# Kernel optimization log

Hardware: AMD Instinct MI355X
Metric: run time of the kernel (lower is better)

## Reference

```python
import jax, jax.numpy as jnp
import numpy as np

NUM_CLASSES = 1203
C = NUM_CLASSES + 1
ITER = 9001            # > warm_up_iter=8000 (full path), not a multiple of save_iter=1000
GAMMA = 1.0
BETA = 1.0             # forward default loss_type=1 -> beta = 1
EMA = 0.999
LOWER = 1.0 / 3.0
UPPER = 5.0
LOSS_WEIGHT_ARG = 1.0  # forward `loss_weight` arg default
SELF_LOSS_WEIGHT = 1.0 # __init__ loss_weight
N = 16384              # multiple of 64 (interval in collect_grad_optim)


def setup_inputs() -> dict:
    key = jax.random.key(0)
    k1, k2, k3, k4, k5 = jax.random.split(key, 5)
    cls_score = jax.random.normal(k1, (N, C), jnp.float32)
    label = jax.random.randint(k2, (N,), 0, C)
    weight = jax.random.uniform(k3, (N,), jnp.float32)
    classes_logits = jax.random.normal(k4, (C,), jnp.float32) * 0.01
    class_weights_buf = jnp.ones((C,), jnp.float32)
    corr_grad_accu = jax.random.normal(k5, (C, C), jnp.float32) * 0.01
    weights_mean = jnp.ones((1,), jnp.float32)
    return {"cls_score": cls_score, "label": label, "weight": weight,
            "classes_logits": classes_logits, "class_weights_buf": class_weights_buf,
            "corr_grad_accu": corr_grad_accu, "weights_mean": weights_mean}


def reference(cls_score, label, weight, classes_logits, class_weights_buf,
              corr_grad_accu, weights_mean):
    sg = jax.lax.stop_gradient
    n = cls_score.shape[0]
    target = jax.nn.one_hot(label, C, dtype=cls_score.dtype)  # expand_label

    # ---- get_weight (no_grad in torch): beta=1, iter % save_iter != 0 ----
    cw = jnp.clip(class_weights_buf, LOWER, UPPER)
    tmp_weight = (cw ** BETA)[label]                 # (class_weights**beta * target).sum(1)
    wm = EMA * weights_mean[0] + (1.0 - EMA) * tmp_weight.mean()
    tmp_weight = tmp_weight / wm
    tmp_weight = sg(tmp_weight * weight)             # detached in torch

    # ---- focal cross-entropy ----
    logp = jax.nn.log_softmax(cls_score, axis=-1)
    CE = -jnp.take_along_axis(logp, label[:, None], axis=1)[:, 0]
    p = jnp.exp(-CE)
    loss = (1.0 - p) ** GAMMA * CE
    loss = (loss * tmp_weight).mean()                # weight_reduce_loss mean

    # ---- collect_grad_optim (all under no_grad in torch) ----
    cs = sg(cls_score)
    w = sg(weight)
    prob = jax.nn.softmax(cs, axis=-1) + 1e-5                       # [N,C]
    focal_grad = w[:, None] * ((1.0 - prob) / prob - jnp.log(prob)) # [N,C]
    pos_grad = ((1.0 - prob) * prob * focal_grad * target).mean(0)  # [C]
    # corr[i,j] = mean_n target[n,i]*focal_grad[n,i]*prob[n,i]*prob[n,j]
    a = target * focal_grad * prob                                  # [N,C]
    corr = jnp.einsum('ni,nj->ij', a, prob) / n                     # [C,C]
    diag = jnp.arange(C)
    corr = corr.at[diag, diag].set(-pos_grad)
    corr_grad = corr * 100.0 * LOSS_WEIGHT_ARG      # dist.all_reduce = identity (1 proc)

    # ITER >= warm_up_iter branch: EMA update + class weights from logits
    accu = EMA * sg(corr_grad_accu) + (1.0 - EMA) * corr_grad
    cw2 = sg(jax.nn.softmax(classes_logits)) * C    # detached in torch

    tcw = (cw2[:, None] * accu).sum(0) / (-jnp.diagonal(accu) + 1e-6) + cw2
    # ITER > warm_up_iter branch:
    tcw = tcw.at[-1].set(C - tcw[:-1].sum())
    tcw = jnp.clip(tcw, LOWER, UPPER)
    tcw = tcw.at[-1].set(jnp.clip(tcw[-1], LOWER, 1.0))
    tcw = sg(jnp.log(tcw))
    loss_grad = ((tcw - classes_logits) ** 2).mean()

    return (SELF_LOSS_WEIGHT * loss, loss_grad, cw2)
```

## Files before the change

kernel.cpp:

```cpp
#include <hip/hip_runtime.h>
#include <math.h>

#define C_  1204
#define C4_ 301
#define NROWBLK 2048

__device__ __forceinline__ float waveReduceSum(float v){
    #pragma unroll
    for (int o = 32; o > 0; o >>= 1) v += __shfl_xor(v, o, 64);
    return v;
}
__device__ __forceinline__ float exp4(float4 v){
    return __expf(v.x) + __expf(v.y) + __expf(v.z) + __expf(v.w);
}
__device__ __forceinline__ float4 accExp(float4 acc, float sc, float4 x){
    acc.x += sc * __expf(x.x); acc.y += sc * __expf(x.y);
    acc.z += sc * __expf(x.z); acc.w += sc * __expf(x.w);
    return acc;
}

__global__ void k_init(float* posg, int* counts, float* tcol){
    int i = blockIdx.x * blockDim.x + threadIdx.x;
    if (i < C_){ posg[i] = 0.f; counts[i] = 0; tcol[i] = 0.f; }
}

__global__ void k_rows(const float* __restrict__ cs, const int* __restrict__ label,
                       const float* __restrict__ w, const float* __restrict__ cwb,
                       float* __restrict__ rowsum, float* __restrict__ aN,
                       float* posg, int* counts,
                       float* __restrict__ part1, float* __restrict__ part2){
    int lane = threadIdx.x & 63;
    int wid  = threadIdx.x >> 6;
    int nA = (blockIdx.x * 4 + wid) * 2;
    int nB = nA + 1;
    const float4* rowA = reinterpret_cast<const float4*>(cs + (size_t)nA * C_);
    const float4* rowB = reinterpret_cast<const float4*>(cs + (size_t)nB * C_);
    bool has4 = lane < (C4_ - 256);

    float4 a0 = rowA[lane], a1 = rowA[lane + 64], a2 = rowA[lane + 128], a3 = rowA[lane + 192];
    float4 b0 = rowB[lane], b1 = rowB[lane + 64], b2 = rowB[lane + 128], b3 = rowB[lane + 192];
    float4 a4, b4;
    if (has4){ a4 = rowA[lane + 256]; b4 = rowB[lane + 256]; }

    float sA = exp4(a0) + exp4(a1) + exp4(a2) + exp4(a3);
    float sB = exp4(b0) + exp4(b1) + exp4(b2) + exp4(b3);
    if (has4){ sA += exp4(a4); sB += exp4(b4); }
    sA = waveReduceSum(sA);
    sB = waveReduceSum(sB);

    __shared__ float lr1[8], lr2[8];
    if (lane < 2){
        int   n = (lane == 0) ? nA : nB;
        float s = (lane == 0) ? sA : sB;
        rowsum[n] = s;
        int l = label[n];
        float x = cs[(size_t)n * C_ + l];
        float logp = x - __logf(s);
        float p = __expf(logp);
        float lossc = (1.f - p) * (-logp);
        float t = fminf(fmaxf(cwb[l], 1.f/3.f), 5.f);
        float wn = w[n];
        float pp = p + 1e-5f;
        float fg = wn * ((1.f - pp) / pp - __logf(pp));
        aN[n] = fg * pp;
        atomicAdd(&posg[l], (1.f - pp) * pp * fg);
        atomicAdd(&counts[l], 1);
        lr1[wid * 2 + lane] = lossc * t * wn;
        lr2[wid * 2 + lane] = t;
    }
    __syncthreads();
    if (threadIdx.x == 0){
        float s1 = 0.f, s2 = 0.f;
        #pragma unroll
        for (int k = 0; k < 8; ++k){ s1 += lr1[k]; s2 += lr2[k]; }
        part1[blockIdx.x] = s1;
        part2[blockIdx.x] = s2;
    }
}

__global__ void k_mid(const int* __restrict__ counts, int* offsets, int* cursor,
                      const float* __restrict__ logits, float* cw2, float* out){
    __shared__ int partial[256];
    __shared__ float red[256];
    int t = threadIdx.x;
    int base = t * 5;
    int local[5]; int s = 0;
    #pragma unroll
    for (int k = 0; k < 5; ++k){
        int idx = base + k;
        int c = (idx < C_) ? counts[idx] : 0;
        local[k] = s; s += c;
    }
    partial[t] = s;
    __syncthreads();
    for (int o = 1; o < 256; o <<= 1){
        int v = 0;
        if (t >= o) v = partial[t - o];
        __syncthreads();
        partial[t] += v;
        __syncthreads();
    }
    int pre = (t > 0) ? partial[t - 1] : 0;
    #pragma unroll
    for (int k = 0; k < 5; ++k){
        int idx = base + k;
        if (idx < C_){ offsets[idx] = pre + local[k]; cursor[idx] = pre + local[k]; }
    }

    float x[5]; float m = -3.402823466e38f;
    #pragma unroll
    for (int k = 0; k < 5; ++k){
        int j = t + k * 256;
        x[k] = (j < C_) ? logits[j] : -3.402823466e38f;
        m = fmaxf(m, x[k]);
    }
    red[t] = m; __syncthreads();
    for (int o = 128; o > 0; o >>= 1){ if (t < o) red[t] = fmaxf(red[t], red[t+o]); __syncthreads(); }
    float bm = red[0]; __syncthreads();
    float ss = 0.f;
    #pragma unroll
    for (int k = 0; k < 5; ++k){ int j = t + k * 256; if (j < C_) ss += __expf(x[k] - bm); }
    red[t] = ss; __syncthreads();
    for (int o = 128; o > 0; o >>= 1){ if (t < o) red[t] += red[t+o]; __syncthreads(); }
    float bs = red[0]; __syncthreads();
    #pragma unroll
    for (int k = 0; k < 5; ++k){
        int j = t + k * 256;
        if (j < C_){ float v = __expf(x[k] - bm) / bs * (float)C_; cw2[j] = v; out[2 + j] = v; }
    }
}

__global__ void k_scatter(const int* __restrict__ label, int* cursor, int* bucket){
    int n = blockIdx.x * blockDim.x + threadIdx.x;
    int l = label[n];
    int pos = atomicAdd(&cursor[l], 1);
    bucket[pos] = n;
}

__global__ void k_corr(const float* __restrict__ cs, const int* __restrict__ bucket,
                       const int* __restrict__ counts, const int* __restrict__ offsets,
                       const float* __restrict__ rowsum, const float* __restrict__ aN,
                       const float* __restrict__ posg, const float* __restrict__ cga,
                       float* __restrict__ accu, int Nn){
    int i = blockIdx.x;
    int t = threadIdx.x;
    int cnt = counts[i], start = offsets[i];
    bool has2 = t < (C4_ - 256);
    float4 acc0 = {0.f,0.f,0.f,0.f}, acc1 = {0.f,0.f,0.f,0.f};
    float suma = 0.f;

    int nbat = (cnt + 7) >> 3;
    for (int b = 0; b < nbat; ++b){
        int s = b << 3;
        #define LOADR(k) \
            int  id##k = min(s + k, cnt - 1); \
            int  n##k  = bucket[start + id##k]; \
            float va##k = aN[n##k]; \
            float iv##k = (s + k < cnt) ? va##k / rowsum[n##k] : 0.f; \
            float ma##k = (s + k < cnt) ? va##k : 0.f; \
            const float4* rp##k = reinterpret_cast<const float4*>(cs + (size_t)n##k * C_); \
            float4 x0##k = rp##k[t]; \
            float4 x1##k; if (has2) x1##k = rp##k[t + 256];
        LOADR(0) LOADR(1) LOADR(2) LOADR(3) LOADR(4) LOADR(5) LOADR(6) LOADR(7)
        #undef LOADR
        suma += ma0 + ma1 + ma2 + ma3 + ma4 + ma5 + ma6 + ma7;
        acc0 = accExp(acc0, iv0, x00); acc0 = accExp(acc0, iv1, x01);
        acc0 = accExp(acc0, iv2, x02); acc0 = accExp(acc0, iv3, x03);
        acc0 = accExp(acc0, iv4, x04); acc0 = accExp(acc0, iv5, x05);
        acc0 = accExp(acc0, iv6, x06); acc0 = accExp(acc0, iv7, x07);
        if (has2){
            acc1 = accExp(acc1, iv0, x10); acc1 = accExp(acc1, iv1, x11);
            acc1 = accExp(acc1, iv2, x12); acc1 = accExp(acc1, iv3, x13);
            acc1 = accExp(acc1, iv4, x14); acc1 = accExp(acc1, iv5, x15);
            acc1 = accExp(acc1, iv6, x16); acc1 = accExp(acc1, iv7, x17);
        }
    }

    float eps   = suma * 1e-5f;
    float scale = 100.f / (float)Nn;
    float diagv = -100.f * posg[i] / (float)Nn;
    const float4* cga4 = reinterpret_cast<const float4*>(cga + (size_t)i * C_);
    float4*       out4 = reinterpret_cast<float4*>(accu + (size_t)i * C_);
    int d4 = i >> 2, dc = i & 3;

    float4 cgv;
    cgv.x = (acc0.x + eps) * scale; cgv.y = (acc0.y + eps) * scale;
    cgv.z = (acc0.z + eps) * scale; cgv.w = (acc0.w + eps) * scale;
    if (t == d4){
        if (dc == 0) cgv.x = diagv; else if (dc == 1) cgv.y = diagv;
        else if (dc == 2) cgv.z = diagv; else cgv.w = diagv;
    }
    float4 gv = cga4[t];
    float4 wv;
    wv.x = 0.999f*gv.x + 0.001f*cgv.x; wv.y = 0.999f*gv.y + 0.001f*cgv.y;
    wv.z = 0.999f*gv.z + 0.001f*cgv.z; wv.w = 0.999f*gv.w + 0.001f*cgv.w;
    out4[t] = wv;

    if (has2){
        int t2 = t + 256;
        float4 cgv1;
        cgv1.x = (acc1.x + eps) * scale; cgv1.y = (acc1.y + eps) * scale;
        cgv1.z = (acc1.z + eps) * scale; cgv1.w = (acc1.w + eps) * scale;
        if (t2 == d4){
            if (dc == 0) cgv1.x = diagv; else if (dc == 1) cgv1.y = diagv;
            else if (dc == 2) cgv1.z = diagv; else cgv1.w = diagv;
        }
        float4 gv1 = cga4[t2];
        float4 wv1;
        wv1.x = 0.999f*gv1.x + 0.001f*cgv1.x; wv1.y = 0.999f*gv1.y + 0.001f*cgv1.y;
        wv1.z = 0.999f*gv1.z + 0.001f*cgv1.z; wv1.w = 0.999f*gv1.w + 0.001f*cgv1.w;
        out4[t2] = wv1;
    }
}

__global__ void k_matvec(const float* __restrict__ cw2, const float* __restrict__ accu,
                         float* tcol){
    int j = blockIdx.x * 256 + threadIdx.x;
    if (j >= C_) return;
    int i0 = blockIdx.y * 32, i1 = min(i0 + 32, C_);
    float p = 0.f;
    #pragma unroll 4
    for (int i = i0; i < i1; ++i) p += cw2[i] * accu[(size_t)i * C_ + j];
    atomicAdd(&tcol[j], p);
}

__global__ void k_final(const float* __restrict__ tcol, const float* __restrict__ accu,
                        const float* __restrict__ cw2, const float* __restrict__ logits,
                        const float* __restrict__ part1, const float* __restrict__ part2,
                        const float* __restrict__ wm0, float* out, int Nn){
    __shared__ float tcw[C_];
    __shared__ float red[256];
    __shared__ float red2[256];
    int t = threadIdx.x;

    float p1 = 0.f, p2 = 0.f;
    for (int k = t; k < NROWBLK; k += 256){ p1 += part1[k]; p2 += part2[k]; }
    red[t] = p1; red2[t] = p2; __syncthreads();
    for (int o = 128; o > 0; o >>= 1){
        if (t < o){ red[t] += red[t+o]; red2[t] += red2[t+o]; }
        __syncthreads();
    }
    float sumLoss = red[0], sumT = red2[0];
    __syncthreads();

    float psum = 0.f;
    #pragma unroll
    for (int k = 0; k < 5; ++k){
        int j = t + k * 256;
        if (j < C_ - 1){
            float denom = -accu[(size_t)j * C_ + j] + 1e-6f;
            float v = tcol[j] / denom + cw2[j];
            tcw[j] = v; psum += v;
        }
    }
    red[t] = psum; __syncthreads();
    for (int o = 128; o > 0; o >>= 1){ if (t < o) red[t] += red[t+o]; __syncthreads(); }
    if (t == 0) tcw[C_ - 1] = (float)C_ - red[0];
    __syncthreads();
    float sq = 0.f;
    #pragma unroll
    for (int k = 0; k < 5; ++k){
        int j = t + k * 256;
        if (j < C_){
            float hi = (j == C_ - 1) ? 1.f : 5.f;
            float v = fminf(fmaxf(tcw[j], 1.f/3.f), hi);
            float d = logf(v) - logits[j];
            sq += d * d;
        }
    }
    red[t] = sq; __syncthreads();
    for (int o = 128; o > 0; o >>= 1){ if (t < o) red[t] += red[t+o]; __syncthreads(); }
    if (t == 0){
        float wm = 0.999f * wm0[0] + 0.001f * (sumT / (float)Nn);
        out[0] = sumLoss / ((float)Nn * wm);
        out[1] = red[0] / (float)C_;
    }
}

extern "C" void kernel_launch(void* const* d_in, const int* in_sizes, int n_in,
                              void* d_out, int out_size, void* d_ws, size_t ws_size,
                              hipStream_t stream){
    (void)n_in; (void)out_size; (void)ws_size;
    const float* cs     = (const float*)d_in[0];
    const int*   label  = (const int*)  d_in[1];
    const float* weight = (const float*)d_in[2];
    const float* logits = (const float*)d_in[3];
    const float* cwb    = (const float*)d_in[4];
    const float* cga    = (const float*)d_in[5];
    const float* wm0    = (const float*)d_in[6];
    float* out = (float*)d_out;
    const int N = in_sizes[1];

    float* ws      = (float*)d_ws;
    float* rowsum  = ws;
    float* aN      = ws + N;
    int*   bucket  = (int*)(ws + 2 * N);
    int*   counts  = (int*)(ws + 3 * N);
    int*   offsets = counts + C_;
    int*   cursor  = offsets + C_;
    float* posg    = (float*)(cursor + C_);
    float* cw2     = posg + C_;
    float* tcol    = cw2 + C_;
    float* part1   = tcol + C_;
    float* part2   = part1 + NROWBLK;
    float* accu    = part2 + NROWBLK;

    k_init    <<<(C_ + 255) / 256, 256, 0, stream>>>(posg, counts, tcol);
    k_rows    <<<NROWBLK,          256, 0, stream>>>(cs, label, weight, cwb, rowsum,
                                                     aN, posg, counts, part1, part2);
    k_mid     <<<1,                256, 0, stream>>>(counts, offsets, cursor, logits, cw2, out);
    k_scatter <<<N / 256,          256, 0, stream>>>(label, cursor, bucket);
    k_corr    <<<C_,               256, 0, stream>>>(cs, bucket, counts, offsets, rowsum,
                                                     aN, posg, cga, accu, N);
    dim3 g4((C_ + 255) / 256, (C_ + 31) / 32);
    k_matvec  <<<g4,               256, 0, stream>>>(cw2, accu, tcol);
    k_final   <<<1,                256, 0, stream>>>(tcol, accu, cw2, logits, part1, part2,
                                                     wm0, out, N);
}
```

Before: 170.7 us.

## Remove global atomics: shared-memory label histogram, per-row diag sums, partial matvec

The label histogram now runs in shared memory inside the single-block mid kernel, so the init kernel and global atomics on counts are gone. Positive-gradient diagonal terms are computed in k_corr from per-row stored probabilities instead of atomics in k_rows. The matvec writes per-chunk partial sums (ten chunks of 128 rows) that the final kernel reduces, which replaces float atomicAdd. The trade-off is a serial histogram over 16K labels inside one block and an extra per-row buffer, but it removes one launch and the atomic contention.

```diff
diff --git a/kernel.cpp b/kernel.cpp
--- a/kernel.cpp
+++ b/kernel.cpp
@@ -1,9 +1,10 @@
 #include <hip/hip_runtime.h>
 #include <math.h>
 
-#define C_  1204
-#define C4_ 301
+#define C_   1204
+#define C4_  301
 #define NROWBLK 2048
+#define NYCHUNK 10
 
 __device__ __forceinline__ float waveReduceSum(float v){
     #pragma unroll
@@ -19,15 +20,77 @@
     return acc;
 }
 
-__global__ void k_init(float* posg, int* counts, float* tcol){
-    int i = blockIdx.x * blockDim.x + threadIdx.x;
-    if (i < C_){ posg[i] = 0.f; counts[i] = 0; tcol[i] = 0.f; }
+__global__ void k_mid(const int* __restrict__ label, int N,
+                      int* offsets, int* cursor,
+                      const float* __restrict__ logits, float* cw2, float* out){
+    __shared__ int hist[C_];
+    __shared__ int partial[256];
+    __shared__ float red[256];
+    int t = threadIdx.x;
+    for (int j = t; j < C_; j += 256) hist[j] = 0;
+    __syncthreads();
+    for (int k = t; k < N; k += 256) atomicAdd(&hist[label[k]], 1);
+    __syncthreads();
+
+    int base = t * 5;
+    int local[5]; int s = 0;
+    #pragma unroll
+    for (int k = 0; k < 5; ++k){
+        int idx = base + k;
+        int c = (idx < C_) ? hist[idx] : 0;
+        local[k] = s; s += c;
+    }
+    partial[t] = s;
+    __syncthreads();
+    for (int o = 1; o < 256; o <<= 1){
+        int v = 0;
+        if (t >= o) v = partial[t - o];
+        __syncthreads();
+        partial[t] += v;
+        __syncthreads();
+    }
+    int pre = (t > 0) ? partial[t - 1] : 0;
+    #pragma unroll
+    for (int k = 0; k < 5; ++k){
+        int idx = base + k;
+        if (idx < C_){ offsets[idx] = pre + local[k]; cursor[idx] = pre + local[k]; }
+    }
+    if (t == 255) offsets[C_] = pre + s;
+
+    float x[5]; float m = -3.402823466e38f;
+    #pragma unroll
+    for (int k = 0; k < 5; ++k){
+        int j = t + k * 256;
+        x[k] = (j < C_) ? logits[j] : -3.402823466e38f;
+        m = fmaxf(m, x[k]);
+    }
+    red[t] = m; __syncthreads();
+    for (int o = 128; o > 0; o >>= 1){ if (t < o) red[t] = fmaxf(red[t], red[t+o]); __syncthreads(); }
+    float bm = red[0]; __syncthreads();
+    float ss = 0.f;
+    #pragma unroll
+    for (int k = 0; k < 5; ++k){ int j = t + k * 256; if (j < C_) ss += __expf(x[k] - bm); }
+    red[t] = ss; __syncthreads();
+    for (int o = 128; o > 0; o >>= 1){ if (t < o) red[t] += red[t+o]; __syncthreads(); }
+    float bs = red[0]; __syncthreads();
+    #pragma unroll
+    for (int k = 0; k < 5; ++k){
+        int j = t + k * 256;
+        if (j < C_){ float v = __expf(x[k] - bm) / bs * (float)C_; cw2[j] = v; out[2 + j] = v; }
+    }
+}
+
+__global__ void k_scatter(const int* __restrict__ label, int* cursor, int* bucket){
+    int n = blockIdx.x * blockDim.x + threadIdx.x;
+    int l = label[n];
+    int pos = atomicAdd(&cursor[l], 1);
+    bucket[pos] = n;
 }
 
 __global__ void k_rows(const float* __restrict__ cs, const int* __restrict__ label,
                        const float* __restrict__ w, const float* __restrict__ cwb,
                        float* __restrict__ rowsum, float* __restrict__ aN,
-                       float* posg, int* counts,
+                       float* __restrict__ pN,
                        float* __restrict__ part1, float* __restrict__ part2){
     int lane = threadIdx.x & 63;
     int wid  = threadIdx.x >> 6;
@@ -63,8 +126,7 @@
         float pp = p + 1e-5f;
         float fg = wn * ((1.f - pp) / pp - __logf(pp));
         aN[n] = fg * pp;
-        atomicAdd(&posg[l], (1.f - pp) * pp * fg);
-        atomicAdd(&counts[l], 1);
+        pN[n] = pp;
         lr1[wid * 2 + lane] = lossc * t * wn;
         lr2[wid * 2 + lane] = t;
     }
@@ -78,76 +140,18 @@
     }
 }
 
-__global__ void k_mid(const int* __restrict__ counts, int* offsets, int* cursor,
-                      const float* __restrict__ logits, float* cw2, float* out){
-    __shared__ int partial[256];
-    __shared__ float red[256];
-    int t = threadIdx.x;
-    int base = t * 5;
-    int local[5]; int s = 0;
-    #pragma unroll
-    for (int k = 0; k < 5; ++k){
-        int idx = base + k;
-        int c = (idx < C_) ? counts[idx] : 0;
-        local[k] = s; s += c;
-    }
-    partial[t] = s;
-    __syncthreads();
-    for (int o = 1; o < 256; o <<= 1){
-        int v = 0;
-        if (t >= o) v = partial[t - o];
-        __syncthreads();
-        partial[t] += v;
-        __syncthreads();
-    }
-    int pre = (t > 0) ? partial[t - 1] : 0;
-    #pragma unroll
-    for (int k = 0; k < 5; ++k){
-        int idx = base + k;
-        if (idx < C_){ offsets[idx] = pre + local[k]; cursor[idx] = pre + local[k]; }
-    }
-
-    float x[5]; float m = -3.402823466e38f;
-    #pragma unroll
-    for (int k = 0; k < 5; ++k){
-        int j = t + k * 256;
-        x[k] = (j < C_) ? logits[j] : -3.402823466e38f;
-        m = fmaxf(m, x[k]);
-    }
-    red[t] = m; __syncthreads();
-    for (int o = 128; o > 0; o >>= 1){ if (t < o) red[t] = fmaxf(red[t], red[t+o]); __syncthreads(); }
-    float bm = red[0]; __syncthreads();
-    float ss = 0.f;
-    #pragma unroll
-    for (int k = 0; k < 5; ++k){ int j = t + k * 256; if (j < C_) ss += __expf(x[k] - bm); }
-    red[t] = ss; __syncthreads();
-    for (int o = 128; o > 0; o >>= 1){ if (t < o) red[t] += red[t+o]; __syncthreads(); }
-    float bs = red[0]; __syncthreads();
-    #pragma unroll
-    for (int k = 0; k < 5; ++k){
-        int j = t + k * 256;
-        if (j < C_){ float v = __expf(x[k] - bm) / bs * (float)C_; cw2[j] = v; out[2 + j] = v; }
-    }
-}
-
-__global__ void k_scatter(const int* __restrict__ label, int* cursor, int* bucket){
-    int n = blockIdx.x * blockDim.x + threadIdx.x;
-    int l = label[n];
-    int pos = atomicAdd(&cursor[l], 1);
-    bucket[pos] = n;
-}
-
 __global__ void k_corr(const float* __restrict__ cs, const int* __restrict__ bucket,
-                       const int* __restrict__ counts, const int* __restrict__ offsets,
+                       const int* __restrict__ offsets,
                        const float* __restrict__ rowsum, const float* __restrict__ aN,
-                       const float* __restrict__ posg, const float* __restrict__ cga,
+                       const float* __restrict__ pN, const float* __restrict__ cga,
                        float* __restrict__ accu, int Nn){
     int i = blockIdx.x;
     int t = threadIdx.x;
-    int cnt = counts[i], start = offsets[i];
+    int start = offsets[i];
+    int cnt   = offsets[i + 1] - start;
     bool has2 = t < (C4_ - 256);
     float4 acc0 = {0.f,0.f,0.f,0.f}, acc1 = {0.f,0.f,0.f,0.f};
-    float suma = 0.f;
+    float suma = 0.f, sumb = 0.f;
 
     int nbat = (cnt + 7) >> 3;
     for (int b = 0; b < nbat; ++b){
@@ -156,6 +160,7 @@
             int  id##k = min(s + k, cnt - 1); \
             int  n##k  = bucket[start + id##k]; \
             float va##k = aN[n##k]; \
+            float pb##k = pN[n##k]; \
             float iv##k = (s + k < cnt) ? va##k / rowsum[n##k] : 0.f; \
             float ma##k = (s + k < cnt) ? va##k : 0.f; \
             const float4* rp##k = reinterpret_cast<const float4*>(cs + (size_t)n##k * C_); \
@@ -164,6 +169,8 @@
         LOADR(0) LOADR(1) LOADR(2) LOADR(3) LOADR(4) LOADR(5) LOADR(6) LOADR(7)
         #undef LOADR
         suma += ma0 + ma1 + ma2 + ma3 + ma4 + ma5 + ma6 + ma7;
+        sumb += ma0*pb0 + ma1*pb1 + ma2*pb2 + ma3*pb3
+              + ma4*pb4 + ma5*pb5 + ma6*pb6 + ma7*pb7;
         acc0 = accExp(acc0, iv0, x00); acc0 = accExp(acc0, iv1, x01);
         acc0 = accExp(acc0, iv2, x02); acc0 = accExp(acc0, iv3, x03);
         acc0 = accExp(acc0, iv4, x04); acc0 = accExp(acc0, iv5, x05);
@@ -178,7 +185,7 @@
 
     float eps   = suma * 1e-5f;
     float scale = 100.f / (float)Nn;
-    float diagv = -100.f * posg[i] / (float)Nn;
+    float diagv = -100.f * (suma - sumb) / (float)Nn;
     const float4* cga4 = reinterpret_cast<const float4*>(cga + (size_t)i * C_);
     float4*       out4 = reinterpret_cast<float4*>(accu + (size_t)i * C_);
     int d4 = i >> 2, dc = i & 3;
@@ -214,17 +221,17 @@
 }
 
 __global__ void k_matvec(const float* __restrict__ cw2, const float* __restrict__ accu,
-                         float* tcol){
+                         float* __restrict__ tpart){
     int j = blockIdx.x * 256 + threadIdx.x;
     if (j >= C_) return;
-    int i0 = blockIdx.y * 32, i1 = min(i0 + 32, C_);
+    int i0 = blockIdx.y * 128, i1 = min(i0 + 128, C_);
     float p = 0.f;
     #pragma unroll 4
     for (int i = i0; i < i1; ++i) p += cw2[i] * accu[(size_t)i * C_ + j];
-    atomicAdd(&tcol[j], p);
-}
-
-__global__ void k_final(const float* __restrict__ tcol, const float* __restrict__ accu,
+    tpart[blockIdx.y * C_ + j] = p;
+}
+
+__global__ void k_final(const float* __restrict__ tpart, const float* __restrict__ accu,
                         const float* __restrict__ cw2, const float* __restrict__ logits,
                         const float* __restrict__ part1, const float* __restrict__ part2,
                         const float* __restrict__ wm0, float* out, int Nn){
@@ -248,8 +255,11 @@
     for (int k = 0; k < 5; ++k){
         int j = t + k * 256;
         if (j < C_ - 1){
+            float tc = 0.f;
+            #pragma unroll
+            for (int y = 0; y < NYCHUNK; ++y) tc += tpart[y * C_ + j];
             float denom = -accu[(size_t)j * C_ + j] + 1e-6f;
-            float v = tcol[j] / denom + cw2[j];
+            float v = tc / denom + cw2[j];
             tcw[j] = v; psum += v;
         }
     }
@@ -294,26 +304,24 @@
     float* ws      = (float*)d_ws;
     float* rowsum  = ws;
     float* aN      = ws + N;
-    int*   bucket  = (int*)(ws + 2 * N);
-    int*   counts  = (int*)(ws + 3 * N);
-    int*   offsets = counts + C_;
-    int*   cursor  = offsets + C_;
-    float* posg    = (float*)(cursor + C_);
-    float* cw2     = posg + C_;
-    float* tcol    = cw2 + C_;
-    float* part1   = tcol + C_;
+    float* pN      = ws + 2 * N;
+    int*   bucket  = (int*)(ws + 3 * N);
+    int*   offsets = (int*)(ws + 4 * N);
+    int*   cursor  = offsets + 1208;
+    float* cw2     = (float*)(cursor + C_);
+    float* part1   = cw2 + C_;
     float* part2   = part1 + NROWBLK;
-    float* accu    = part2 + NROWBLK;
-
-    k_init    <<<(C_ + 255) / 256, 256, 0, stream>>>(posg, counts, tcol);
-    k_rows    <<<NROWBLK,          256, 0, stream>>>(cs, label, weight, cwb, rowsum,
-                                                     aN, posg, counts, part1, part2);
-    k_mid     <<<1,                256, 0, stream>>>(counts, offsets, cursor, logits, cw2, out);
-    k_scatter <<<N / 256,          256, 0, stream>>>(label, cursor, bucket);
-    k_corr    <<<C_,               256, 0, stream>>>(cs, bucket, counts, offsets, rowsum,
-                                                     aN, posg, cga, accu, N);
-    dim3 g4((C_ + 255) / 256, (C_ + 31) / 32);
-    k_matvec  <<<g4,               256, 0, stream>>>(cw2, accu, tcol);
-    k_final   <<<1,                256, 0, stream>>>(tcol, accu, cw2, logits, part1, part2,
-                                                     wm0, out, N);
-}
+    float* tpart   = part2 + NROWBLK;
+    float* accu    = tpart + NYCHUNK * C_;
+
+    k_mid     <<<1,        256, 0, stream>>>(label, N, offsets, cursor, logits, cw2, out);
+    k_scatter <<<N / 256,  256, 0, stream>>>(label, cursor, bucket);
+    k_rows    <<<NROWBLK,  256, 0, stream>>>(cs, label, weight, cwb, rowsum, aN, pN,
+                                             part1, part2);
+    k_corr    <<<C_,       256, 0, stream>>>(cs, bucket, offsets, rowsum, aN, pN,
+                                             cga, accu, N);
+    dim3 g4((C_ + 255) / 256, NYCHUNK);
+    k_matvec  <<<g4,       256, 0, stream>>>(cw2, accu, tpart);
+    k_final   <<<1,        256, 0, stream>>>(tpart, accu, cw2, logits, part1, part2,
+                                             wm0, out, N);
+}
```

Measured after the change: 190.7 us. 1.12x slower.
